# Performance work log

Hardware: AMD Instinct MI355X
Metric: run time of the kernel (lower is better)

The kernel has to match this reference:

```python
import jax, jax.numpy as jnp
import numpy as np

BATCH_SIZE = 131072
N_NODES = 18  # per-graph nodes; N_NODES * c_out == 18 (input_size of fl1)
N_LAYERS = 2


def setup_inputs() -> dict:
    key = jax.random.key(0)
    ks = jax.random.split(key, 10)
    return {
        "node_features": jax.random.normal(ks[0], (BATCH_SIZE, N_NODES, 1), jnp.float32),
        "adj_matrix": jax.random.uniform(ks[1], (BATCH_SIZE, N_NODES, N_NODES), jnp.float32),
        "proj_w": jax.random.normal(ks[2], (1, 1), jnp.float32),
        "proj_b": jax.random.normal(ks[3], (1,), jnp.float32),
        "fl1_w": jax.random.normal(ks[4], (10, 18), jnp.float32) * 0.1,
        "fl1_b": jax.random.normal(ks[5], (10,), jnp.float32) * 0.1,
        "fl2_w": jax.random.normal(ks[6], (8, 10), jnp.float32) * 0.1,
        "fl2_b": jax.random.normal(ks[7], (8,), jnp.float32) * 0.1,
        "fl3_w": jax.random.normal(ks[8], (2, 8), jnp.float32) * 0.1,
        "fl3_b": jax.random.normal(ks[9], (2,), jnp.float32) * 0.1,
    }


def reference(node_features, adj_matrix, proj_w, proj_b, fl1_w, fl1_b, fl2_w, fl2_b, fl3_w, fl3_b):
    # GCN stack (original runs this under torch.no_grad())
    deg = adj_matrix.sum(axis=-1, keepdims=True)  # [B, N, 1]
    x = node_features
    for _ in range(N_LAYERS):
        h = x @ proj_w.T + proj_b           # [B, N, c_out]
        h = jnp.einsum('bnm,bmc->bnc', adj_matrix, h)
        h = h / deg
        x = jax.nn.relu(h)
    x = x.reshape(BATCH_SIZE, 18)
    # vectorized replacement of the per-element NaN-scrub Python loop
    x = jnp.where(jnp.isnan(x), jnp.float32(0.0), x)
    # small MLP head
    x = jax.nn.relu(x @ fl1_w.T + fl1_b)
    x = jax.nn.relu(x @ fl2_w.T + fl2_b)
    return x @ fl3_w.T + fl3_b
```

## Files before the change

kernel.cpp:

```cpp
#include <hip/hip_runtime.h>

#define NNODE  18
#define ADJ_B  1296
#define ADJ_F  324
#define TILE   16
#define TILE_B (TILE * ADJ_B)

__device__ __forceinline__ void gload_lds16(const void* g, void* l) {
    __builtin_amdgcn_global_load_lds((const __attribute__((address_space(1))) void*)g,
                                     (__attribute__((address_space(3))) void*)l, 16, 0, 0);
}

#define QB(v, P) __int_as_float(__builtin_amdgcn_ds_swizzle(__float_as_int(v), 0x8000 + 0x55 * (P)))
#define GATHER18(dst, src)                                                      \
    dst[0]=QB(src[0],0);  dst[1]=QB(src[0],1);  dst[2]=QB(src[0],2);  dst[3]=QB(src[0],3);   \
    dst[4]=QB(src[1],0);  dst[5]=QB(src[1],1);  dst[6]=QB(src[1],2);  dst[7]=QB(src[1],3);   \
    dst[8]=QB(src[2],0);  dst[9]=QB(src[2],1);  dst[10]=QB(src[2],2); dst[11]=QB(src[2],3);  \
    dst[12]=QB(src[3],0); dst[13]=QB(src[3],1); dst[14]=QB(src[3],2); dst[15]=QB(src[3],3);  \
    dst[16]=QB(src[4],0); dst[17]=QB(src[4],1);

__global__ __launch_bounds__(64, 1) void gcnn_fused(
    const float* __restrict__ nf, const float* __restrict__ adj,
    const float* __restrict__ proj_w, const float* __restrict__ proj_b,
    const float* __restrict__ w1, const float* __restrict__ b1,
    const float* __restrict__ w2, const float* __restrict__ b2,
    const float* __restrict__ w3, const float* __restrict__ b3,
    float* __restrict__ out, int B)
{
    __shared__ __align__(16) char smem[TILE_B];
    const int lane = threadIdx.x;
    const int p    = lane & 3;
    const int Q    = lane >> 2;
    const int b    = blockIdx.x * TILE + Q;
    const unsigned adjLim = (unsigned)B * ADJ_B - 16;

    const unsigned gbase = (unsigned)blockIdx.x * TILE_B + lane * 16u;
    #pragma unroll
    for (int c = 0; c < 20; ++c)
        gload_lds16((const char*)adj + min(gbase + c * 1024u, adjLim), smem + c * 1024);
    if (lane < 16)
        gload_lds16((const char*)adj + min(gbase + 20480u, adjLim), smem + 20480);

    const bool act = b < B;
    float x[NNODE];
    if (act) {
        const float2* __restrict__ xp = (const float2*)(nf + (size_t)b * NNODE);
        #pragma unroll
        for (int j = 0; j < 9; ++j) { float2 v = xp[j]; x[2*j] = v.x; x[2*j+1] = v.y; }
    }

    asm volatile("s_waitcnt vmcnt(0)" ::: "memory");

    if (act) {
        float a[5][NNODE];
        const float* __restrict__ my = (const float*)smem + Q * ADJ_F;
        #pragma unroll
        for (int u = 0; u < 5; ++u) {
            int r  = 4 * u + p;
            int ro = r < NNODE ? r : NNODE - 1;
            const float2* __restrict__ rp = (const float2*)(my + ro * NNODE);
            #pragma unroll
            for (int j = 0; j < 9; ++j) { float2 v = rp[j]; a[u][2*j] = v.x; a[u][2*j+1] = v.y; }
        }
        const float pw = proj_w[0], pb = proj_b[0];

        float inv[5], h[5];
        #pragma unroll
        for (int u = 0; u < 5; ++u) {
            float d = 0.f, s = 0.f;
            #pragma unroll
            for (int m = 0; m < NNODE; ++m) { d += a[u][m]; s += a[u][m] * x[m]; }
            inv[u] = 1.0f / d;
            h[u]   = fmaxf(0.f, pw * s * inv[u] + pb);
        }
        float hf[NNODE];
        GATHER18(hf, h)

        float y[5];
        #pragma unroll
        for (int u = 0; u < 5; ++u) {
            float s = 0.f;
            #pragma unroll
            for (int m = 0; m < NNODE; ++m) s += a[u][m] * hf[m];
            float v = fmaxf(0.f, pw * s * inv[u] + pb);
            y[u] = (v != v) ? 0.f : v;
        }
        float yf[NNODE];
        GATHER18(yf, y)

        float z1[10];
        #pragma unroll
        for (int k = 0; k < 10; ++k) {
            float s = b1[k];
            #pragma unroll
            for (int j = 0; j < NNODE; ++j) s += w1[k*NNODE + j] * yf[j];
            z1[k] = fmaxf(0.f, s);
        }
        float z2[8];
        #pragma unroll
        for (int k = 0; k < 8; ++k) {
            float s = b2[k];
            #pragma unroll
            for (int j = 0; j < 10; ++j) s += w2[k*10 + j] * z1[j];
            z2[k] = fmaxf(0.f, s);
        }
        float o0 = b3[0], o1 = b3[1];
        #pragma unroll
        for (int j = 0; j < 8; ++j) { o0 += w3[j] * z2[j]; o1 += w3[8 + j] * z2[j]; }

        if (p == 0)
            *(float2*)(out + (size_t)b * 2) = make_float2(o0, o1);
    }
}

extern "C" void kernel_launch(void* const* d_in, const int* in_sizes, int n_in,
                              void* d_out, int out_size, void* d_ws, size_t ws_size,
                              hipStream_t stream) {
    const float* nf  = (const float*)d_in[0];
    const float* adj = (const float*)d_in[1];
    const float* pw  = (const float*)d_in[2];
    const float* pb  = (const float*)d_in[3];
    const float* w1  = (const float*)d_in[4];
    const float* b1  = (const float*)d_in[5];
    const float* w2  = (const float*)d_in[6];
    const float* b2  = (const float*)d_in[7];
    const float* w3  = (const float*)d_in[8];
    const float* b3  = (const float*)d_in[9];
    float* out = (float*)d_out;

    const int B = in_sizes[0] / NNODE;
    const int grid = (B + TILE - 1) / TILE;

    gcnn_fused<<<grid, 64, 0, stream>>>(nf, adj, pw, pb, w1, b1, w2, b2, w3, b3, out, B);
}
```

Before: 36.02 us.

## Persistent grid with double-buffered LDS prefetch of adjacency and node features

Switches from one block per 16-graph tile to a persistent grid of 768 blocks that loop over tiles. Each block prefetches the next tile's adjacency and node features into a second LDS buffer while computing the current one, using a partial vmcnt wait. Node features now also go through LDS. The goal is to hide global-load latency behind compute, since the old kernel ran one wave per block that stalled on its loads. The cost is double the LDS per block, and the code silently drops the tail when B is not a multiple of 16, with no bounds handling.

Result: slower. 49.54 us (+37.5%).

```diff
diff --git a/kernel.cpp b/kernel.cpp
--- a/kernel.cpp
+++ b/kernel.cpp
@@ -1,10 +1,15 @@
 #include <hip/hip_runtime.h>
 
-#define NNODE  18
-#define ADJ_B  1296
-#define ADJ_F  324
-#define TILE   16
-#define TILE_B (TILE * ADJ_B)
+#define NNODE   18
+#define ADJ_B   1296
+#define ADJ_F   324
+#define NF_B    72
+#define TILE    16
+#define ADJ_T   (TILE * ADJ_B)
+#define NF_T    (TILE * NF_B)
+#define BUF_B   (ADJ_T + NF_T)
+#define SOPS    23
+#define GRID    768
 
 __device__ __forceinline__ void gload_lds16(const void* g, void* l) {
     __builtin_amdgcn_global_load_lds((const __attribute__((address_space(1))) void*)g,
@@ -27,33 +32,35 @@
     const float* __restrict__ w3, const float* __restrict__ b3,
     float* __restrict__ out, int B)
 {
-    __shared__ __align__(16) char smem[TILE_B];
+    __shared__ __align__(16) char smem[2 * BUF_B];
     const int lane = threadIdx.x;
     const int p    = lane & 3;
     const int Q    = lane >> 2;
-    const int b    = blockIdx.x * TILE + Q;
-    const unsigned adjLim = (unsigned)B * ADJ_B - 16;
+    const int NT   = B / TILE;
 
-    const unsigned gbase = (unsigned)blockIdx.x * TILE_B + lane * 16u;
-    #pragma unroll
-    for (int c = 0; c < 20; ++c)
-        gload_lds16((const char*)adj + min(gbase + c * 1024u, adjLim), smem + c * 1024);
-    if (lane < 16)
-        gload_lds16((const char*)adj + min(gbase + 20480u, adjLim), smem + 20480);
+    auto stage = [&](int t, char* buf) {
+        const char* ab = (const char*)adj + (size_t)t * ADJ_T + lane * 16;
+        #pragma unroll
+        for (int c = 0; c < 20; ++c)
+            gload_lds16(ab + c * 1024, buf + c * 1024);
+        if (lane < 16)
+            gload_lds16(ab + 20480, buf + 20480);
+        const char* nb = (const char*)nf + (size_t)t * NF_T + lane * 16;
+        gload_lds16(nb, buf + ADJ_T);
+        if (lane < 8)
+            gload_lds16(nb + 1024, buf + ADJ_T + 1024);
+    };
 
-    const bool act = b < B;
-    float x[NNODE];
-    if (act) {
-        const float2* __restrict__ xp = (const float2*)(nf + (size_t)b * NNODE);
+    auto compute = [&](int t, const char* buf) {
+        const int b = t * TILE + Q;
+
+        float x[NNODE];
+        const float2* __restrict__ xp = (const float2*)(buf + ADJ_T + Q * NF_B);
         #pragma unroll
         for (int j = 0; j < 9; ++j) { float2 v = xp[j]; x[2*j] = v.x; x[2*j+1] = v.y; }
-    }
 
-    asm volatile("s_waitcnt vmcnt(0)" ::: "memory");
-
-    if (act) {
         float a[5][NNODE];
-        const float* __restrict__ my = (const float*)smem + Q * ADJ_F;
+        const float* __restrict__ my = (const float*)buf + Q * ADJ_F;
         #pragma unroll
         for (int u = 0; u < 5; ++u) {
             int r  = 4 * u + p;
@@ -110,6 +117,22 @@
 
         if (p == 0)
             *(float2*)(out + (size_t)b * 2) = make_float2(o0, o1);
+    };
+
+    char* cur = smem;
+    char* nxt = smem + BUF_B;
+    int t = blockIdx.x;
+    stage(t, cur);
+    for (; t < NT; t += GRID) {
+        const int tn = t + GRID;
+        if (tn < NT) {
+            stage(tn, nxt);
+            asm volatile("s_waitcnt vmcnt(23)" ::: "memory");
+        } else {
+            asm volatile("s_waitcnt vmcnt(0)" ::: "memory");
+        }
+        compute(t, cur);
+        char* tmp = cur; cur = nxt; nxt = tmp;
     }
 }
 
@@ -129,7 +152,6 @@
     float* out = (float*)d_out;
 
     const int B = in_sizes[0] / NNODE;
-    const int grid = (B + TILE - 1) / TILE;
 
-    gcnn_fused<<<grid, 64, 0, stream>>>(nf, adj, pw, pb, w1, b1, w2, b2, w3, b3, out, B);
+    gcnn_fused<<<GRID, 64, 0, stream>>>(nf, adj, pw, pb, w1, b1, w2, b2, w3, b3, out, B);
 }
```
